# Performance work log

Hardware: AMD Instinct MI355X
Metric: run time of the kernel (lower is better)

Reference implementation:

```python
import jax, jax.numpy as jnp
import numpy as np

N_NODES = 50000
N_EDGES = 800000
IN, HID, OUT = 128, 256, 128
BN_EPS = 1e-5

def setup_inputs() -> dict:
    key = jax.random.key(0)
    ks = jax.random.split(key, 16)
    def lin(k, fan_in, shape):
        b = 1.0 / np.sqrt(fan_in)
        return jax.random.uniform(k, shape, jnp.float32, -b, b)
    return {
        "node_feat": jax.random.normal(ks[0], (N_NODES, IN), jnp.float32),
        "coord_feat": jax.random.normal(ks[1], (N_NODES, 3), jnp.float32),
        "src": jax.random.randint(ks[2], (N_EDGES,), 0, N_NODES, jnp.int32),
        "dst": jax.random.randint(ks[3], (N_EDGES,), 0, N_NODES, jnp.int32),
        "W_e1": lin(ks[4], 2 * IN + 1, (2 * IN + 1, HID)),
        "b_e1": jnp.zeros((HID,), jnp.float32),
        "W_e2": lin(ks[5], HID, (HID, HID)),
        "b_e2": jnp.zeros((HID,), jnp.float32),
        "W_c1": lin(ks[6], HID, (HID, HID)),
        "b_c1": jnp.zeros((HID,), jnp.float32),
        "W_c2": lin(ks[7], HID, (HID, 1)),
        "W_n1": lin(ks[8], IN + HID, (IN + HID, HID)),
        "b_n1": jnp.zeros((HID,), jnp.float32),
        "W_n2": lin(ks[9], HID, (HID, OUT)),
        "b_n2": jnp.zeros((OUT,), jnp.float32),
        "gamma": jnp.ones((OUT,), jnp.float32),
        "beta": jnp.zeros((OUT,), jnp.float32),
    }

def reference(node_feat, coord_feat, src, dst, W_e1, b_e1, W_e2, b_e2,
              W_c1, b_c1, W_c2, W_n1, b_n1, W_n2, b_n2, gamma, beta):
    silu = jax.nn.silu
    # per-edge geometry (DGL u_sub_v: src - dst)
    x_diff = coord_feat[src] - coord_feat[dst]              # [E, 3]
    radial = jnp.sum(jnp.square(x_diff), axis=1, keepdims=True)  # [E, 1]
    x_diff = x_diff / (jnp.sqrt(radial) + 1e-30)
    # edge MLP on gathered features
    f = jnp.concatenate([node_feat[src], node_feat[dst], radial], axis=-1)  # [E, 2*IN+1]
    msg_h = silu(silu(f @ W_e1 + b_e1) @ W_e2 + b_e2)       # [E, HID]
    # coord message
    msg_x = (silu(msg_h @ W_c1 + b_c1) @ W_c2) * x_diff     # [E, 3]
    # aggregate at destination nodes
    h_neigh = jax.ops.segment_sum(msg_h, dst, num_segments=N_NODES)  # sum
    x_sum = jax.ops.segment_sum(msg_x, dst, num_segments=N_NODES)
    deg = jax.ops.segment_sum(jnp.ones((msg_x.shape[0],), msg_x.dtype), dst,
                              num_segments=N_NODES)
    x_neigh = x_sum / jnp.maximum(deg, 1.0)[:, None]        # mean; 0 for isolated nodes
    # node MLP + BatchNorm (training-mode batch stats, biased var)
    h = silu(jnp.concatenate([node_feat, h_neigh], axis=-1) @ W_n1 + b_n1) @ W_n2 + b_n2
    mu = jnp.mean(h, axis=0)
    var = jnp.mean(jnp.square(h - mu), axis=0)
    h = (h - mu) * jax.lax.rsqrt(var + BN_EPS) * gamma + beta
    x = coord_feat + x_neigh
    return h, x
```

## Files before the change

### kernel.cpp

```cpp
#include <hip/hip_runtime.h>
#include <stdint.h>

typedef unsigned short u16;
typedef __bf16 bf16x8 __attribute__((ext_vector_type(8)));
typedef unsigned short u16x8 __attribute__((ext_vector_type(8)));
typedef float f32x4 __attribute__((ext_vector_type(4)));

#define N_NODES 50000
#define N_EDGES 800000

enum : uint32_t {
  WS_WT_E1 = 0u,
  WS_WT_E2 = 131072u,
  WS_WT_C1 = 262144u,
  WS_WT_N1 = 393216u,
  WS_WT_N2 = 589824u,
  WS_WRAD  = 655360u,
  WS_WC2   = 656384u,
  WS_B_E1  = 657408u,
  WS_B_E2  = 658432u,
  WS_B_C1  = 659456u,
  WS_B_N1  = 660480u,
  WS_B_N2  = 661504u,
  WS_GAMMA = 662016u,
  WS_BETA  = 662528u,
  WS_SCALE = 663040u,
  WS_SHIFT = 663552u,
  WS_STAT  = 664064u,
  WS_FLAG  = 665600u,
  WS_DEG   = 1048576u,
  WS_OFF   = 1248576u,
  WS_BSUM  = 1448704u,
  WS_BPRE  = 1449728u,
  WS_CUR   = 1450752u,
  WS_EID   = 1650752u,
  WS_XSUM  = 4850752u,
  WS_CF    = 5450752u,
  WS_NF    = 6050752u,
  WS_HN    = 18850752u,
  WS_PA    = 70050752u,
  WS_PB    = 95675328u,
  WS_PRE_END = 121299904u
};

__device__ __forceinline__ float b2f(u16 u){ uint32_t x=((uint32_t)u)<<16; float f; __builtin_memcpy(&f,&x,4); return f; }
__device__ __forceinline__ u16 f2b(float f){ __bf16 h = (__bf16)f; return __builtin_bit_cast(unsigned short, h); }
__device__ __forceinline__ float silu_f(float x){
  return x * __builtin_amdgcn_rcpf(1.0f + __expf(-x));
}
__device__ __forceinline__ float ldin(const void* p, int i, int fl){
  return fl ? ((const float*)p)[i] : b2f(((const u16*)p)[i]);
}

__global__ void detect_k(const void* nf, int* flag){
  if (threadIdx.x == 0){
    const u16* p = (const u16*)nf;
    int cnt = 0;
    for (int i=0;i<128;i++){
      u16 u = p[2*i];
      int e = (u >> 7) & 0xFF;
      if (e >= 0x90) cnt++;
    }
    *flag = (cnt >= 8) ? 1 : 0;
  }
}

__global__ void cvt_nf_k(const void* nf, char* ws, const int* flagp){
  int fl = *flagp;
  int i = blockIdx.x*256 + threadIdx.x;
  if (i >= (N_NODES*128)/4) return;
  ushort4* out = (ushort4*)(ws + WS_NF);
  if (fl){
    const float4* p = (const float4*)nf;
    float4 v = p[i];
    ushort4 o; o.x=f2b(v.x); o.y=f2b(v.y); o.z=f2b(v.z); o.w=f2b(v.w);
    out[i] = o;
  } else {
    out[i] = ((const ushort4*)nf)[i];
  }
}

__global__ void cvt_cf_k(const void* cd, char* ws, const int* flagp){
  int fl = *flagp;
  int i = blockIdx.x*256 + threadIdx.x;
  if (i >= N_NODES*3) return;
  ((float*)(ws + WS_CF))[i] = ldin(cd, i, fl);
}

__global__ void prep_k(const void* We1, const void* be1, const void* We2, const void* be2,
                       const void* Wc1, const void* bc1, const void* Wc2,
                       const void* Wn1, const void* bn1, const void* Wn2, const void* bn2,
                       const void* gam, const void* bet, char* ws, const int* flagp)
{
  int fl = *flagp;
  int g = blockIdx.x*256 + threadIdx.x;
  if (g < 65536){ int n=g>>8,k=g&255; ((u16*)(ws+WS_WT_E1))[n*256+k]=f2b(ldin(We1,k*256+n,fl)); return; } g-=65536;
  if (g < 65536){
    int j=g&7, l=(g>>3)&63, nblk=(g>>9)&15, kk=g>>13;
    int n=nblk*16+(l&15), k=kk*32+((l>>4)&3)*8+j;
    ((u16*)(ws+WS_WT_E2))[g]=f2b(ldin(We2,k*256+n,fl)); return; } g-=65536;
  if (g < 65536){
    int j=g&7, l=(g>>3)&63, nblk=(g>>9)&15, kk=g>>13;
    int n=nblk*16+(l&15), k=kk*32+((l>>4)&3)*8+j;
    ((u16*)(ws+WS_WT_C1))[g]=f2b(ldin(Wc1,k*256+n,fl)); return; } g-=65536;
  if (g < 98304){ int n=g/384,k=g-n*384; ((u16*)(ws+WS_WT_N1))[n*384+k]=f2b(ldin(Wn1,k*256+n,fl)); return; } g-=98304;
  if (g < 32768){ int n=g>>8,k=g&255; ((u16*)(ws+WS_WT_N2))[n*256+k]=f2b(ldin(Wn2,k*128+n,fl)); return; } g-=32768;
  if (g < 256){ ((float*)(ws+WS_WRAD))[g]=ldin(We1,65536+g,fl); return; } g-=256;
  if (g < 256){ ((float*)(ws+WS_WC2))[g]=ldin(Wc2,g,fl); return; } g-=256;
  if (g < 256){ ((float*)(ws+WS_B_E1))[g]=ldin(be1,g,fl); return; } g-=256;
  if (g < 256){ ((float*)(ws+WS_B_E2))[g]=ldin(be2,g,fl); return; } g-=256;
  if (g < 256){ ((float*)(ws+WS_B_C1))[g]=ldin(bc1,g,fl); return; } g-=256;
  if (g < 256){ ((float*)(ws+WS_B_N1))[g]=ldin(bn1,g,fl); return; } g-=256;
  if (g < 128){ ((float*)(ws+WS_B_N2))[g]=ldin(bn2,g,fl); return; } g-=128;
  if (g < 128){ ((float*)(ws+WS_GAMMA))[g]=ldin(gam,g,fl); return; } g-=128;
  if (g < 128){ ((float*)(ws+WS_BETA))[g]=ldin(bet,g,fl); return; }
}

__global__ void histo_k(const int* __restrict__ dst, int* __restrict__ deg){
  int e = blockIdx.x*256 + threadIdx.x;
  if (e < N_EDGES) atomicAdd(&deg[dst[e]], 1);
}

__global__ void scanA_k(const int* __restrict__ deg, int* __restrict__ off, int* __restrict__ bsum){
  int t = threadIdx.x; int i = blockIdx.x*256 + t;
  int lane = t & 63, w = t >> 6;
  int v = (i < N_NODES) ? deg[i] : 0;
  int x = v;
  #pragma unroll
  for (int d=1; d<64; d<<=1){ int o = __shfl_up(x, d, 64); if (lane >= d) x += o; }
  __shared__ int wt[4];
  if (lane == 63) wt[w] = x;
  __syncthreads();
  int add = 0;
  if (w > 0) add += wt[0];
  if (w > 1) add += wt[1];
  if (w > 2) add += wt[2];
  x += add;
  if (i < N_NODES) off[i] = x;
  if (t == 255) bsum[blockIdx.x] = x;
}

__global__ void scanB_k(const int* __restrict__ bsum, int* __restrict__ bpre, int* __restrict__ off){
  int t = threadIdx.x;
  int lane = t & 63, w = t >> 6;
  int v = (t < 196) ? bsum[t] : 0;
  int x = v;
  #pragma unroll
  for (int d=1; d<64; d<<=1){ int o = __shfl_up(x, d, 64); if (lane >= d) x += o; }
  __shared__ int wt[4];
  if (lane == 63) wt[w] = x;
  __syncthreads();
  int add = 0;
  if (w > 0) add += wt[0];
  if (w > 1) add += wt[1];
  if (w > 2) add += wt[2];
  x += add;
  if (t < 196) bpre[t] = x - v;
  if (t == 255) off[N_NODES] = x;
}

__global__ void scanC_k(const int* __restrict__ deg, int* __restrict__ off,
                        const int* __restrict__ bpre, int* __restrict__ cur){
  int i = blockIdx.x*256 + threadIdx.x;
  if (i >= N_NODES) return;
  int excl = off[i] - deg[i] + bpre[blockIdx.x];
  off[i] = excl; cur[i] = excl;
}

__global__ void scatter_k(const int* __restrict__ dst, int* __restrict__ cur, int* __restrict__ eid){
  int e = blockIdx.x*256 + threadIdx.x;
  if (e >= N_EDGES) return;
  int p = atomicAdd(&cur[dst[e]], 1);
  eid[p] = e;
}

__global__ __launch_bounds__(512, 4) void pab_k(const u16* __restrict__ nfc,
                                                const char* __restrict__ wsw,
                                                u16* __restrict__ pa, u16* __restrict__ pb)
{
  const int t = threadIdx.x, lane = t & 63, wid = t >> 6;
  const int mw = wid & 1, nw = wid >> 1;
  const int mbase = mw << 6, nbase = nw << 6;
  const int l15 = lane & 15, l4 = lane >> 4;
  const int tile = blockIdx.x;
  const int sel  = blockIdx.y;
  const u16* Wt = (const u16*)(wsw + WS_WT_E1);
  const float* b1 = (const float*)(wsw + WS_B_E1);
  u16* out = sel ? pb : pa;

  f32x4 acc[4][4];
  #pragma unroll
  for (int mi=0;mi<4;mi++)
  #pragma unroll
  for (int ni=0;ni<4;ni++){ float b_ = sel ? 0.f : b1[nbase+ni*16+l15]; acc[mi][ni]=(f32x4){b_,b_,b_,b_}; }

  #pragma unroll
  for (int kk=0;kk<4;kk++){
    const int kel = kk*32 + l4*8;
    bf16x8 av[4];
    #pragma unroll
    for (int mi=0;mi<4;mi++){
      int row = tile*128 + mbase + mi*16 + l15;
      if (row >= N_NODES) row = 0;
      av[mi] = *(const bf16x8*)(nfc + (size_t)row*128 + kel);
    }
    #pragma unroll
    for (int ni=0;ni<4;ni++){
      int n_ = nbase + ni*16 + l15;
      bf16x8 bv = *(const bf16x8*)(Wt + (size_t)n_*256 + sel*128 + kel);
      #pragma unroll
      for (int mi=0;mi<4;mi++)
        acc[mi][ni] = __builtin_amdgcn_mfma_f32_16x16x32_bf16(av[mi], bv, acc[mi][ni], 0,0,0);
    }
  }
  #pragma unroll
  for (int mi=0;mi<4;mi++)
  #pragma unroll
  for (int ni=0;ni<4;ni++)
  #pragma unroll
  for (int j=0;j<4;j++){
    int m_ = tile*128 + mbase + mi*16 + l4*4 + j;
    if (m_ < N_NODES){
      int n_ = nbase + ni*16 + l15;
      out[(size_t)m_*256 + n_] = f2b(acc[mi][ni][j]);
    }
  }
}

#define FRAG_GEMM4(FB, BIAS_L) do { \
  _Pragma("unroll") for (int mi=0;mi<4;mi++) _Pragma("unroll") for (int ni=0;ni<4;ni++){ \
    float b_ = BIAS_L[nbase + ni*16 + l15]; acc[mi][ni] = (f32x4){b_,b_,b_,b_}; } \
  _Pragma("unroll") for (int kk=0;kk<8;kk++){ \
    const int kel = kk*32 + l4*8; \
    bf16x8 av[4]; \
    _Pragma("unroll") for (int mi=0;mi<4;mi++){ \
      int row = mbase + mi*16 + l15; \
      uint32_t byte = ((uint32_t)row<<9) ^ ((uint32_t)kel<<1) ^ ((uint32_t)(row&7)<<4); \
      av[mi] = *(const bf16x8*)((const char*)h_lds + byte); \
    } \
    _Pragma("unroll") for (int ni=0;ni<4;ni++){ \
      bf16x8 bv = *(const bf16x8*)(FB + (((kk<<4) + nblk0 + ni)<<9) + lane*8); \
      _Pragma("unroll") for (int mi=0;mi<4;mi++) \
        acc[mi][ni] = __builtin_amdgcn_mfma_f32_16x16x32_bf16(av[mi], bv, acc[mi][ni], 0,0,0); \
    } \
  } } while(0)

#define SILU_STORE4() do { \
  _Pragma("unroll") for (int mi=0;mi<4;mi++) _Pragma("unroll") for (int ni=0;ni<4;ni++) \
  _Pragma("unroll") for (int j=0;j<4;j++){ \
    int m_ = mbase + mi*16 + l4*4 + j; int n_ = nbase + ni*16 + l15; \
    float v_ = silu_f(acc[mi][ni][j]); \
    uint32_t byte = ((uint32_t)m_<<9) ^ ((uint32_t)n_<<1) ^ ((uint32_t)(m_&7)<<4); \
    *(u16*)((char*)h_lds + byte) = f2b(v_); \
  } } while(0)

template<bool PRE>
__global__ __launch_bounds__(512, 4) void edge_mlp(
    const u16* __restrict__ nfc, const float* __restrict__ coord,
    const int* __restrict__ src, const int* __restrict__ dst,
    const char* __restrict__ wsw, const int* __restrict__ eid,
    const u16* __restrict__ pa, const u16* __restrict__ pb,
    float* __restrict__ h_neigh, float* __restrict__ xsum)
{
  __shared__ u16 h_lds[32768];
  __shared__ int s_ids[128], d_ids[128];
  __shared__ float rad_l[128], xd_l[128][3];
  __shared__ float cpart[4][128];
  __shared__ float b1_l[256], b2_l[256], b3_l[256], wc2_l[256];

  const int t = threadIdx.x, lane = t & 63, wid = t >> 6;
  const int mw = wid & 1, nw = wid >> 1;
  const int mbase = mw << 6, nbase = nw << 6;
  const int nblk0 = nw << 2;
  const int l15 = lane & 15, l4 = lane >> 4;
  const int tile = blockIdx.x;

  const u16* FB2 = (const u16*)(wsw + WS_WT_E2);
  const u16* FB3 = (const u16*)(wsw + WS_WT_C1);

  if (t < 128) {
    int e = eid[tile*128 + t];
    int s = src[e], d = dst[e];
    s_ids[t] = s; d_ids[t] = d;
    float ax = coord[s*3+0]-coord[d*3+0];
    float ay = coord[s*3+1]-coord[d*3+1];
    float az = coord[s*3+2]-coord[d*3+2];
    float r2 = ax*ax+ay*ay+az*az;
    float inv = 1.0f/(sqrtf(r2) + 1e-30f);
    rad_l[t] = r2; xd_l[t][0]=ax*inv; xd_l[t][1]=ay*inv; xd_l[t][2]=az*inv;
  }
  if (t >= 128 && t < 384) {
    int c = t - 128;
    b1_l[c]  = ((const float*)(wsw+WS_B_E1))[c];
    b2_l[c]  = ((const float*)(wsw+WS_B_E2))[c];
    b3_l[c]  = ((const float*)(wsw+WS_B_C1))[c];
    wc2_l[c] = ((const float*)(wsw+WS_WC2))[c];
  }
  __syncthreads();

  f32x4 acc[4][4];

  if constexpr (PRE) {
    const int r1 = t >> 2, cq = (t & 3) << 6;
    const int s1 = s_ids[r1], d1 = d_ids[r1];
    const float rr = rad_l[r1];
    const u16* par = pa + (size_t)s1*256 + cq;
    const u16* pbr = pb + (size_t)d1*256 + cq;
    const float* wrg = (const float*)(wsw + WS_WRAD) + cq;
    #pragma unroll
    for (int q=0;q<8;q++){
      u16x8 ua = *(const u16x8*)(par + q*8);
      u16x8 ub = *(const u16x8*)(pbr + q*8);
      f32x4 w0 = *(const f32x4*)(wrg + q*8);
      f32x4 w1 = *(const f32x4*)(wrg + q*8 + 4);
      u16x8 o;
      #pragma unroll
      for (int j=0;j<8;j++){
        float wv = (j<4) ? w0[j] : w1[j-4];
        float hv = silu_f(b2f(ua[j]) + b2f(ub[j]) + rr*wv);
        o[j] = f2b(hv);
      }
      int c = cq + q*8;
      uint32_t byte = ((uint32_t)r1<<9) ^ ((uint32_t)c<<1) ^ ((uint32_t)(r1&7)<<4);
      *(u16x8*)((char*)h_lds + byte) = o;
    }
  } else {
    #pragma unroll
    for (int mi=0;mi<4;mi++)
    #pragma unroll
    for (int ni=0;ni<4;ni++){ float b_ = b1_l[nbase+ni*16+l15]; acc[mi][ni]=(f32x4){b_,b_,b_,b_}; }
    const u16* Wt1 = (const u16*)(wsw + WS_WT_E1);
    #pragma unroll
    for (int kk=0;kk<8;kk++){
      const int kel = kk*32 + l4*8;
      bf16x8 av[4];
      #pragma unroll
      for (int mi=0;mi<4;mi++){
        int row = mbase + mi*16 + l15;
        int nid = (kk < 4) ? s_ids[row] : d_ids[row];
        int k = (kk < 4) ? kel : (kel - 128);
        av[mi] = *(const bf16x8*)(nfc + (size_t)nid*128 + k);
      }
      #pragma unroll
      for (int ni=0;ni<4;ni++){
        int n_ = nbase + ni*16 + l15;
        bf16x8 bv = *(const bf16x8*)(Wt1 + (size_t)n_*256 + kel);
        #pragma unroll
        for (int mi=0;mi<4;mi++)
          acc[mi][ni] = __builtin_amdgcn_mfma_f32_16x16x32_bf16(av[mi], bv, acc[mi][ni], 0,0,0);
      }
    }
    #pragma unroll
    for (int mi=0;mi<4;mi++)
    #pragma unroll
    for (int ni=0;ni<4;ni++){
      int n_ = nbase + ni*16 + l15;
      float wrn = ((const float*)(wsw+WS_WRAD))[n_];
      #pragma unroll
      for (int j=0;j<4;j++){
        int m_ = mbase + mi*16 + l4*4 + j;
        float v_ = silu_f(acc[mi][ni][j] + rad_l[m_]*wrn);
        uint32_t byte = ((uint32_t)m_<<9) ^ ((uint32_t)n_<<1) ^ ((uint32_t)(m_&7)<<4);
        *(u16*)((char*)h_lds + byte) = f2b(v_);
      }
    }
  }
  __syncthreads();

  FRAG_GEMM4(FB2, b2_l);
  __syncthreads();
  SILU_STORE4();
  __syncthreads();

  FRAG_GEMM4(FB3, b3_l);
  float part[4][4];
  #pragma unroll
  for (int mi=0;mi<4;mi++)
  #pragma unroll
  for (int j=0;j<4;j++) part[mi][j] = 0.f;
  #pragma unroll
  for (int mi=0;mi<4;mi++)
  #pragma unroll
  for (int ni=0;ni<4;ni++){
    int n_ = nbase + ni*16 + l15;
    float w = wc2_l[n_];
    #pragma unroll
    for (int j=0;j<4;j++) part[mi][j] += silu_f(acc[mi][ni][j]) * w;
  }
  #pragma unroll
  for (int off_=1; off_<16; off_<<=1)
  #pragma unroll
  for (int mi=0;mi<4;mi++)
  #pragma unroll
  for (int j=0;j<4;j++) part[mi][j] += __shfl_xor(part[mi][j], off_, 64);
  if (l15 == 0){
    #pragma unroll
    for (int mi=0;mi<4;mi++)
    #pragma unroll
    for (int j=0;j<4;j++){
      int m_ = mbase + mi*16 + l4*4 + j;
      cpart[nw][m_] = part[mi][j];
    }
  }
  __syncthreads();

  if (t < 128){
    float csum = cpart[0][t] + cpart[1][t] + cpart[2][t] + cpart[3][t];
    int dd = d_ids[t];
    float v0 = csum*xd_l[t][0], v1 = csum*xd_l[t][1], v2 = csum*xd_l[t][2];
    #pragma unroll
    for (int off_=1; off_<64; off_<<=1){
      float u0=__shfl_up(v0,off_,64), u1=__shfl_up(v1,off_,64), u2=__shfl_up(v2,off_,64);
      int du=__shfl_up(dd,off_,64);
      if (lane >= off_ && du == dd){ v0+=u0; v1+=u1; v2+=u2; }
    }
    int dn = __shfl_down(dd,1,64);
    if (lane == 63 || dn != dd){
      unsafeAtomicAdd(&xsum[dd*3+0], v0);
      unsafeAtomicAdd(&xsum[dd*3+1], v1);
      unsafeAtomicAdd(&xsum[dd*3+2], v2);
    }
  }
  {
    int col  = t & 255;
    int half = t >> 8;
    int rb   = half << 6;
    float a2 = 0.f; int prev = d_ids[rb]; bool firstrun = true;
    #pragma unroll
    for (int ii=0; ii<64; ii+=8){
      float v[8]; int dv[8];
      #pragma unroll
      for (int j=0;j<8;j++){
        int m_ = rb + ii + j;
        uint32_t byte = ((uint32_t)m_<<9) ^ ((uint32_t)col<<1) ^ ((uint32_t)(m_&7)<<4);
        v[j] = b2f(*(const u16*)((const char*)h_lds + byte));
        dv[j] = d_ids[m_];
      }
      #pragma unroll
      for (int j=0;j<8;j++){
        if (dv[j] != prev){
          float* p = &h_neigh[(size_t)prev*256 + col];
          if (firstrun) unsafeAtomicAdd(p, a2); else *p = a2;
          firstrun = false; a2 = v[j]; prev = dv[j];
        } else a2 += v[j];
      }
    }
    unsafeAtomicAdd(&h_neigh[(size_t)prev*256 + col], a2);
  }
}

__global__ void x_out_k(const float* __restrict__ coord, const int* __restrict__ deg,
                        const float* __restrict__ xsum, void* __restrict__ d_out,
                        const int* __restrict__ flagp)
{
  int fl = *flagp;
  int n = blockIdx.x*256 + threadIdx.x;
  if (n >= N_NODES) return;
  float dm = fmaxf((float)deg[n], 1.f);
  float v0 = coord[n*3+0] + xsum[n*3+0]/dm;
  float v1 = coord[n*3+1] + xsum[n*3+1]/dm;
  float v2 = coord[n*3+2] + xsum[n*3+2]/dm;
  const size_t base = (size_t)N_NODES*128 + (size_t)n*3;
  if (fl){
    float* o = (float*)d_out;
    o[base+0]=v0; o[base+1]=v1; o[base+2]=v2;
  } else {
    u16* o = (u16*)d_out;
    o[base+0]=f2b(v0); o[base+1]=f2b(v1); o[base+2]=f2b(v2);
  }
}

#define SILU_STORE8() do { \
  _Pragma("unroll") for (int mi=0;mi<8;mi++) _Pragma("unroll") for (int ni=0;ni<4;ni++) \
  _Pragma("unroll") for (int j=0;j<4;j++){ \
    int m_ = mbase + mi*16 + l4*4 + j; int n_ = nbase + ni*16 + l15; \
    float v_ = silu_f(acc[mi][ni][j]); \
    uint32_t byte = ((uint32_t)m_<<9) ^ ((uint32_t)n_<<1) ^ ((uint32_t)(m_&7)<<4); \
    *(u16*)((char*)h_lds + byte) = f2b(v_); \
  } } while(0)

__global__ __launch_bounds__(512, 2) void node_mlp(
    const u16* __restrict__ node_feat, const float* __restrict__ h_neigh,
    const char* __restrict__ wsw, u16* __restrict__ hpre)
{
  __shared__ u16 h_lds[65536];
  __shared__ float b1_l[256], b2_l[128];

  const int t = threadIdx.x, lane = t & 63, wid = t >> 6;
  const int mw = wid & 1, nw = wid >> 1;
  const int mbase = mw << 7, nbase = nw << 6;
  const int l15 = lane & 15, l4 = lane >> 4;
  const int tile = blockIdx.x;

  if (t < 256) b1_l[t] = ((const float*)(wsw+WS_B_N1))[t];
  if (t < 128) b2_l[t] = ((const float*)(wsw+WS_B_N2))[t];
  __syncthreads();

  const u16* Wt1 = (const u16*)(wsw + WS_WT_N1);
  const u16* Wt2 = (const u16*)(wsw + WS_WT_N2);

  f32x4 acc[8][4];
  #pragma unroll
  for (int mi=0;mi<8;mi++)
  #pragma unroll
  for (int ni=0;ni<4;ni++){ float b_ = b1_l[nbase+ni*16+l15]; acc[mi][ni] = (f32x4){b_,b_,b_,b_}; }

  #pragma unroll
  for (int kk=0;kk<12;kk++){
    const int kel = kk*32 + l4*8;
    bf16x8 av[8];
    #pragma unroll
    for (int mi=0;mi<8;mi++){
      int row = tile*256 + mbase + mi*16 + l15;
      if (row >= N_NODES) row = 0;
      if (kk < 4){
        av[mi] = *(const bf16x8*)(node_feat + (size_t)row*128 + kel);
      } else {
        const float* hp = h_neigh + (size_t)row*256 + (kel - 128);
        u16x8 u;
        #pragma unroll
        for (int e2=0;e2<8;e2++) u[e2] = f2b(hp[e2]);
        av[mi] = __builtin_bit_cast(bf16x8, u);
      }
    }
    #pragma unroll
    for (int ni=0;ni<4;ni++){
      int n_ = nbase + ni*16 + l15;
      bf16x8 bv = *(const bf16x8*)(Wt1 + (size_t)n_*384 + kel);
      #pragma unroll
      for (int mi=0;mi<8;mi++)
        acc[mi][ni] = __builtin_amdgcn_mfma_f32_16x16x32_bf16(av[mi], bv, acc[mi][ni], 0,0,0);
    }
  }
  SILU_STORE8();
  __syncthreads();

  const int nb2 = nw << 5;
  f32x4 acc2[8][2];
  #pragma unroll
  for (int mi=0;mi<8;mi++)
  #pragma unroll
  for (int ni=0;ni<2;ni++){ float b_ = b2_l[nb2+ni*16+l15]; acc2[mi][ni] = (f32x4){b_,b_,b_,b_}; }
  #pragma unroll
  for (int kk=0;kk<8;kk++){
    const int kel = kk*32 + l4*8;
    bf16x8 av[8];
    #pragma unroll
    for (int mi=0;mi<8;mi++){
      int row = mbase + mi*16 + l15;
      uint32_t byte = ((uint32_t)row<<9) ^ ((uint32_t)kel<<1) ^ ((uint32_t)(row&7)<<4);
      av[mi] = *(const bf16x8*)((const char*)h_lds + byte);
    }
    #pragma unroll
    for (int ni=0;ni<2;ni++){
      int n_ = nb2 + ni*16 + l15;
      bf16x8 bv = *(const bf16x8*)(Wt2 + (size_t)n_*256 + kel);
      #pragma unroll
      for (int mi=0;mi<8;mi++)
        acc2[mi][ni] = __builtin_amdgcn_mfma_f32_16x16x32_bf16(av[mi], bv, acc2[mi][ni], 0,0,0);
    }
  }
  #pragma unroll
  for (int mi=0;mi<8;mi++)
  #pragma unroll
  for (int ni=0;ni<2;ni++)
  #pragma unroll
  for (int j=0;j<4;j++){
    int m_ = tile*256 + mbase + mi*16 + l4*4 + j;
    if (m_ < N_NODES){
      int n_ = nb2 + ni*16 + l15;
      hpre[(size_t)m_*128 + n_] = f2b(acc2[mi][ni][j]);
    }
  }
}

__global__ void bn_stats_k(const u16* __restrict__ hpre, float* __restrict__ stat){
  int c = threadIdx.x;
  float s = 0.f, s2 = 0.f;
  for (int r = blockIdx.x; r < N_NODES; r += 256){
    float v = b2f(hpre[(size_t)r*128 + c]);
    s += v; s2 += v*v;
  }
  atomicAdd(&stat[c], s);
  atomicAdd(&stat[128+c], s2);
}

__global__ void bn_final_k(const float* __restrict__ stat, const char* __restrict__ wsw,
                           float* __restrict__ scale, float* __restrict__ shift){
  int c = threadIdx.x;
  if (c >= 128) return;
  float mu = stat[c] * (1.0f/N_NODES);
  float var = stat[128+c] * (1.0f/N_NODES) - mu*mu;
  float rs = rsqrtf(var + 1e-5f);
  float g = ((const float*)(wsw+WS_GAMMA))[c];
  float b = ((const float*)(wsw+WS_BETA))[c];
  scale[c] = rs*g;
  shift[c] = b - mu*rs*g;
}

__global__ void bn_apply_k(const u16* __restrict__ hpre, const float* __restrict__ scale,
                           const float* __restrict__ shift, void* __restrict__ d_out,
                           const int* __restrict__ flagp){
  int fl = *flagp;
  int i = blockIdx.x*256 + threadIdx.x;
  if (i >= N_NODES*128/8) return;
  u16x8 v = *(const u16x8*)(hpre + (size_t)i*8);
  int c0 = (i*8) & 127;
  if (fl){
    float* o = (float*)d_out + (size_t)i*8;
    #pragma unroll
    for (int j=0;j<8;j++) o[j] = b2f(v[j])*scale[c0+j] + shift[c0+j];
  } else {
    u16x8 w;
    #pragma unroll
    for (int j=0;j<8;j++) w[j] = f2b(b2f(v[j])*scale[c0+j] + shift[c0+j]);
    *(u16x8*)((u16*)d_out + (size_t)i*8) = w;
  }
}

extern "C" void kernel_launch(void* const* d_in, const int* in_sizes, int n_in,
                              void* d_out, int out_size, void* d_ws, size_t ws_size,
                              hipStream_t stream)
{
  const void* node_feat_raw = d_in[0];
  const void* coord_raw     = d_in[1];
  const int* src       = (const int*)d_in[2];
  const int* dst       = (const int*)d_in[3];
  char* ws = (char*)d_ws;

  int*   flag  = (int*)(ws + WS_FLAG);
  int*   deg   = (int*)(ws + WS_DEG);
  int*   off   = (int*)(ws + WS_OFF);
  int*   bsum  = (int*)(ws + WS_BSUM);
  int*   bpre  = (int*)(ws + WS_BPRE);
  int*   cur   = (int*)(ws + WS_CUR);
  int*   eid   = (int*)(ws + WS_EID);
  float* xsum  = (float*)(ws + WS_XSUM);
  float* hn    = (float*)(ws + WS_HN);
  u16*   pa    = (u16*)(ws + WS_PA);
  u16*   pb    = (u16*)(ws + WS_PB);
  u16*   hpre  = (u16*)(ws + WS_PA);
  const u16*   nfc = (const u16*)(ws + WS_NF);
  const float* cfc = (const float*)(ws + WS_CF);
  float* stat  = (float*)(ws + WS_STAT);
  float* scale = (float*)(ws + WS_SCALE);
  float* shift = (float*)(ws + WS_SHIFT);

  const bool pre = (ws_size >= (size_t)WS_PRE_END);

  hipMemsetAsync(deg, 0, N_NODES*sizeof(int), stream);
  hipMemsetAsync(xsum, 0, N_NODES*3*sizeof(float), stream);
  hipMemsetAsync(hn, 0, (size_t)N_NODES*256*sizeof(float), stream);
  hipMemsetAsync(stat, 0, 256*sizeof(float), stream);

  detect_k<<<1,64,0,stream>>>(node_feat_raw, flag);
  cvt_nf_k<<<(N_NODES*128/4 + 255)/256,256,0,stream>>>(node_feat_raw, ws, flag);
  cvt_cf_k<<<(N_NODES*3 + 255)/256,256,0,stream>>>(coord_raw, ws, flag);
  prep_k<<<1288,256,0,stream>>>(d_in[4],d_in[5],d_in[6],d_in[7],d_in[8],d_in[9],
                                d_in[10],d_in[11],d_in[12],d_in[13],d_in[14],
                                d_in[15],d_in[16], ws, flag);
  histo_k<<<3125,256,0,stream>>>(dst, deg);
  scanA_k<<<196,256,0,stream>>>(deg, off, bsum);
  scanB_k<<<1,256,0,stream>>>(bsum, bpre, off);
  scanC_k<<<196,256,0,stream>>>(deg, off, bpre, cur);
  scatter_k<<<3125,256,0,stream>>>(dst, cur, eid);

  if (pre){
    pab_k<<<dim3(391,2),512,0,stream>>>(nfc, ws, pa, pb);
    edge_mlp<true><<<6250,512,0,stream>>>(nfc, cfc, src, dst, ws, eid, pa, pb, hn, xsum);
  } else {
    edge_mlp<false><<<6250,512,0,stream>>>(nfc, cfc, src, dst, ws, eid, pa, pb, hn, xsum);
  }

  x_out_k<<<196,256,0,stream>>>(cfc, deg, xsum, d_out, flag);
  node_mlp<<<196,512,0,stream>>>(nfc, hn, ws, hpre);
  bn_stats_k<<<256,128,0,stream>>>(hpre, stat);
  bn_final_k<<<1,128,0,stream>>>(stat, ws, scale, shift);
  bn_apply_k<<<3125,256,0,stream>>>(hpre, scale, shift, d_out, flag);
}
```

Before: 940.9 us.

## Replace fp32 atomic h_neigh aggregation with bf16 stores plus boundary fixup kernel

Edges are sorted by destination, so each half-tile of 64 edges writes its interior segment sums directly as bf16, and its first and last partial segments go into per-half-tile partial buffers. A new per-node fixup kernel then sums those boundary partials. This removes the fp32 atomics, halves the h_neigh memset and reads, and lets node_mlp load bf16 directly. Tiles are also remapped so each XCD handles a contiguous range of edges. The cost is an extra 50000-block launch and some boundary-partial traffic.

```diff
diff --git a/kernel.cpp b/kernel.cpp
--- a/kernel.cpp
+++ b/kernel.cpp
@@ -28,6 +28,8 @@
   WS_SHIFT = 663552u,
   WS_STAT  = 664064u,
   WS_FLAG  = 665600u,
+  WS_PFDA  = 666624u,
+  WS_PFDB  = 716624u,
   WS_DEG   = 1048576u,
   WS_OFF   = 1248576u,
   WS_BSUM  = 1448704u,
@@ -38,6 +40,8 @@
   WS_CF    = 5450752u,
   WS_NF    = 6050752u,
   WS_HN    = 18850752u,
+  WS_PFVA  = 44450752u,
+  WS_PFVB  = 57250752u,
   WS_PA    = 70050752u,
   WS_PB    = 95675328u,
   WS_PRE_END = 121299904u
@@ -260,7 +264,9 @@
     const int* __restrict__ src, const int* __restrict__ dst,
     const char* __restrict__ wsw, const int* __restrict__ eid,
     const u16* __restrict__ pa, const u16* __restrict__ pb,
-    float* __restrict__ h_neigh, float* __restrict__ xsum)
+    u16* __restrict__ hnb, float* __restrict__ xsum,
+    int* __restrict__ pfdA, int* __restrict__ pfdB,
+    float* __restrict__ pfvA, float* __restrict__ pfvB)
 {
   __shared__ u16 h_lds[32768];
   __shared__ int s_ids[128], d_ids[128];
@@ -273,7 +279,10 @@
   const int mbase = mw << 6, nbase = nw << 6;
   const int nblk0 = nw << 2;
   const int l15 = lane & 15, l4 = lane >> 4;
-  const int tile = blockIdx.x;
+
+  const int orig = blockIdx.x;
+  const int xcd = orig & 7;
+  const int tile = (xcd < 2 ? xcd*782 : 2*782 + (xcd-2)*781) + (orig >> 3);
 
   const u16* FB2 = (const u16*)(wsw + WS_WT_E2);
   const u16* FB3 = (const u16*)(wsw + WS_WT_C1);
@@ -425,6 +434,7 @@
     int col  = t & 255;
     int half = t >> 8;
     int rb   = half << 6;
+    int h    = tile*2 + half;
     float a2 = 0.f; int prev = d_ids[rb]; bool firstrun = true;
     #pragma unroll
     for (int ii=0; ii<64; ii+=8){
@@ -439,14 +449,41 @@
       #pragma unroll
       for (int j=0;j<8;j++){
         if (dv[j] != prev){
-          float* p = &h_neigh[(size_t)prev*256 + col];
-          if (firstrun) unsafeAtomicAdd(p, a2); else *p = a2;
-          firstrun = false; a2 = v[j]; prev = dv[j];
+          if (firstrun){
+            pfvA[(size_t)h*256 + col] = a2;
+            if (col == 0) pfdA[h] = prev;
+            firstrun = false;
+          } else {
+            hnb[(size_t)prev*256 + col] = f2b(a2);
+          }
+          a2 = v[j]; prev = dv[j];
         } else a2 += v[j];
       }
     }
-    unsafeAtomicAdd(&h_neigh[(size_t)prev*256 + col], a2);
-  }
+    pfvB[(size_t)h*256 + col] = a2;
+    if (col == 0){
+      pfdB[h] = prev;
+      if (firstrun) pfdA[h] = -1;
+    }
+  }
+}
+
+__global__ void fixup_k(const int* __restrict__ off,
+                        const int* __restrict__ pfdA, const int* __restrict__ pfdB,
+                        const float* __restrict__ pfvA, const float* __restrict__ pfvB,
+                        u16* __restrict__ hnb)
+{
+  int n = blockIdx.x;
+  int c = threadIdx.x;
+  int o0 = off[n], o1 = off[n+1];
+  if (o0 >= o1) return;
+  int h0 = o0 >> 6, h1 = (o1 - 1) >> 6;
+  float s = 0.f; bool touched = false;
+  for (int h = h0; h <= h1; ++h){
+    if (pfdA[h] == n){ s += pfvA[(size_t)h*256 + c]; touched = true; }
+    if (pfdB[h] == n){ s += pfvB[(size_t)h*256 + c]; touched = true; }
+  }
+  if (touched) hnb[(size_t)n*256 + c] = f2b(s);
 }
 
 __global__ void x_out_k(const float* __restrict__ coord, const int* __restrict__ deg,
@@ -480,7 +517,7 @@
   } } while(0)
 
 __global__ __launch_bounds__(512, 2) void node_mlp(
-    const u16* __restrict__ node_feat, const float* __restrict__ h_neigh,
+    const u16* __restrict__ node_feat, const u16* __restrict__ hnb,
     const char* __restrict__ wsw, u16* __restrict__ hpre)
 {
   __shared__ u16 h_lds[65536];
@@ -516,11 +553,7 @@
       if (kk < 4){
         av[mi] = *(const bf16x8*)(node_feat + (size_t)row*128 + kel);
       } else {
-        const float* hp = h_neigh + (size_t)row*256 + (kel - 128);
-        u16x8 u;
-        #pragma unroll
-        for (int e2=0;e2<8;e2++) u[e2] = f2b(hp[e2]);
-        av[mi] = __builtin_bit_cast(bf16x8, u);
+        av[mi] = *(const bf16x8*)(hnb + (size_t)row*256 + (kel - 128));
       }
     }
     #pragma unroll
@@ -636,7 +669,11 @@
   int*   cur   = (int*)(ws + WS_CUR);
   int*   eid   = (int*)(ws + WS_EID);
   float* xsum  = (float*)(ws + WS_XSUM);
-  float* hn    = (float*)(ws + WS_HN);
+  u16*   hnb   = (u16*)(ws + WS_HN);
+  int*   pfdA  = (int*)(ws + WS_PFDA);
+  int*   pfdB  = (int*)(ws + WS_PFDB);
+  float* pfvA  = (float*)(ws + WS_PFVA);
+  float* pfvB  = (float*)(ws + WS_PFVB);
   u16*   pa    = (u16*)(ws + WS_PA);
   u16*   pb    = (u16*)(ws + WS_PB);
   u16*   hpre  = (u16*)(ws + WS_PA);
@@ -650,7 +687,7 @@
 
   hipMemsetAsync(deg, 0, N_NODES*sizeof(int), stream);
   hipMemsetAsync(xsum, 0, N_NODES*3*sizeof(float), stream);
-  hipMemsetAsync(hn, 0, (size_t)N_NODES*256*sizeof(float), stream);
+  hipMemsetAsync(hnb, 0, (size_t)N_NODES*256*sizeof(u16), stream);
   hipMemsetAsync(stat, 0, 256*sizeof(float), stream);
 
   detect_k<<<1,64,0,stream>>>(node_feat_raw, flag);
@@ -667,13 +704,16 @@
 
   if (pre){
     pab_k<<<dim3(391,2),512,0,stream>>>(nfc, ws, pa, pb);
-    edge_mlp<true><<<6250,512,0,stream>>>(nfc, cfc, src, dst, ws, eid, pa, pb, hn, xsum);
+    edge_mlp<true><<<6250,512,0,stream>>>(nfc, cfc, src, dst, ws, eid, pa, pb,
+                                          hnb, xsum, pfdA, pfdB, pfvA, pfvB);
   } else {
-    edge_mlp<false><<<6250,512,0,stream>>>(nfc, cfc, src, dst, ws, eid, pa, pb, hn, xsum);
-  }
-
+    edge_mlp<false><<<6250,512,0,stream>>>(nfc, cfc, src, dst, ws, eid, pa, pb,
+                                           hnb, xsum, pfdA, pfdB, pfvA, pfvB);
+  }
+
+  fixup_k<<<N_NODES,256,0,stream>>>(off, pfdA, pfdB, pfvA, pfvB, hnb);
   x_out_k<<<196,256,0,stream>>>(cfc, deg, xsum, d_out, flag);
-  node_mlp<<<196,512,0,stream>>>(nfc, hn, ws, hpre);
+  node_mlp<<<196,512,0,stream>>>(nfc, hnb, ws, hpre);
   bn_stats_k<<<256,128,0,stream>>>(hpre, stat);
   bn_final_k<<<1,128,0,stream>>>(stat, ws, scale, shift);
   bn_apply_k<<<3125,256,0,stream>>>(hpre, scale, shift, d_out, flag);
```

New measurement: 963.5 us. 1.02x slower.
